# Optimization experiments

Measured on AMD Instinct MI355X. Metric: run time of the kernel, lower is better.

Reference implementation:

```python
import jax, jax.numpy as jnp
import numpy as np

KSIZE = 9
SIGMA = 7.0
ALPHA = 0.05
POOL = 7


def _conv(x, w, pad):
    # x: (N, Cin, H, W), w: (Cout, Cin, kh, kw), zero padding, stride 1
    return jax.lax.conv_general_dilated(
        x, w, window_strides=(1, 1), padding=[(pad, pad), (pad, pad)],
        dimension_numbers=("NCHW", "OIHW", "NCHW"))


def setup_inputs() -> dict:
    key = jax.random.key(0)
    x = jax.random.normal(key, (4, 1, 2048, 2048), dtype=jnp.float32)
    # Sobel filters (ImageGradientsLayer): out ch 0 = Ix, out ch 1 = Iy
    sobel_w = jnp.array(
        [[[[-1., 0., 1.], [-2., 0., 2.], [-1., 0., 1.]]],
         [[[-1., -2., -1.], [0., 0., 0.], [1., 2., 1.]]]], dtype=jnp.float32)
    # Normalized 2D Gaussian kernel, ksize=9, sigma=7
    ax = np.arange(KSIZE) - (KSIZE - 1) / 2.0
    g1 = np.exp(-(ax ** 2) / (2.0 * SIGMA ** 2))
    g2 = np.outer(g1, g1)
    g2 = g2 / g2.sum()
    gauss_w = jnp.asarray(g2, dtype=jnp.float32)[None, None]  # (1,1,9,9)
    return {"x": x, "sobel_w": sobel_w, "gauss_w": gauss_w}


def reference(x, sobel_w, gauss_w):
    # 1) ImageGradientsLayer: Sobel conv -> (N, 2, H, W)
    g = _conv(x, sobel_w, 1)
    Ix, Iy = g[:, 0], g[:, 1]
    # 2) ChannelProductLayer: I_xx, I_yy, I_xy -> (N, 3, H, W)
    prods = jnp.stack([Ix * Ix, Iy * Iy, Ix * Iy], axis=1)
    # 3) SecondMomentMatrixLayer: same 9x9 Gaussian on each channel
    N, C, H, W = prods.shape
    S = _conv(prods.reshape(N * C, 1, H, W), gauss_w, (KSIZE - 1) // 2)
    S = S.reshape(N, C, H, W)
    # 4) CornerResponseLayer: R = det - alpha * trace^2
    det = S[:, 0] * S[:, 1] - S[:, 2] * S[:, 2]
    tr = S[:, 0] + S[:, 1]
    R = (det - ALPHA * tr * tr)[:, None]  # (N, 1, H, W)
    # 5) NMSLayer: global (lower) median threshold, 7x7 maxpool, equality mask
    n = R.size
    med = jnp.sort(R.reshape(-1))[(n - 1) // 2]  # torch.median = lower median
    xt = jnp.where(R > med, R, jnp.zeros_like(R))
    pad = (POOL - 1) // 2
    y = jax.lax.reduce_window(
        xt, -jnp.inf, jax.lax.max, (1, 1, POOL, POOL), (1, 1, 1, 1),
        [(0, 0), (0, 0), (pad, pad), (pad, pad)])
    mask = (xt == y).astype(xt.dtype)
    return mask * xt
```

## Files before the change

### kernel.cpp

```cpp
#include <hip/hip_runtime.h>
#include <cstdint>
#include <math.h>

#define IMH 2048
#define IMW 2048
#define NB 4
#define NPIX (NB*IMH*IMW)
#define MEDRANK ((NPIX-1)/2)
#define ALPHA 0.05f

#define TW 64
#define TH 32

__device__ __forceinline__ uint32_t fkey(float f){
  uint32_t u = __float_as_uint(f);
  return (u & 0x80000000u) ? ~u : (u | 0x80000000u);
}

__device__ __forceinline__ float ldz(const float* __restrict__ p, int r, int c){
  return (r >= 0 && r < IMH && c >= 0 && c < IMW) ? p[(size_t)r*IMW + c] : 0.f;
}

__global__ __launch_bounds__(256) void front_kernel(
    const float* __restrict__ x, const float* __restrict__ sobel_w,
    const float* __restrict__ gauss_w, float* __restrict__ R)
{
  __shared__ float xs[TH+10][TW+16];
  __shared__ float ps[3][TH+8][TW+16];
  __shared__ float hs[TH+8][TW];

  const int tid = threadIdx.x;
  const int C0 = blockIdx.x * TW;
  const int R0 = blockIdx.y * TH;
  const int n  = blockIdx.z;
  const float* xb = x + (size_t)n * (size_t)(IMH*IMW);

  float w0[9], w1[9];
#pragma unroll
  for (int i = 0; i < 9; i++){ w0[i] = sobel_w[i]; w1[i] = sobel_w[9+i]; }
  float ga[9];
  {
    float a4 = sqrtf(gauss_w[4*9+4]);
#pragma unroll
    for (int i = 0; i < 9; i++) ga[i] = gauss_w[4*9+i] / a4;
  }

  for (int u = tid; u < (TH+10)*20; u += 256){
    int r  = u / 20, c4 = u % 20;
    int gr = R0 - 5 + r;
    int gc = C0 - 8 + c4*4;
    float4 v;
    if (gr >= 0 && gr < IMH && gc >= 0 && gc + 3 < IMW){
      v = *reinterpret_cast<const float4*>(&xb[(size_t)gr*IMW + gc]);
    } else {
      v.x = ldz(xb, gr, gc+0);
      v.y = ldz(xb, gr, gc+1);
      v.z = ldz(xb, gr, gc+2);
      v.w = ldz(xb, gr, gc+3);
    }
    *reinterpret_cast<float4*>(&xs[r][c4*4]) = v;
  }
  __syncthreads();

  for (int u = tid; u < (TH+8)*18; u += 256){
    int r  = u / 18;
    int c4 = u % 18 + 1;
    int cb = c4*4;
    int gr = R0 - 4 + r;
    float rw[3][12];
#pragma unroll
    for (int i = 0; i < 3; i++){
      float4 a = *reinterpret_cast<const float4*>(&xs[r+i][cb-4]);
      float4 b = *reinterpret_cast<const float4*>(&xs[r+i][cb]);
      float4 c = *reinterpret_cast<const float4*>(&xs[r+i][cb+4]);
      rw[i][0]=a.x; rw[i][1]=a.y; rw[i][2]=a.z; rw[i][3]=a.w;
      rw[i][4]=b.x; rw[i][5]=b.y; rw[i][6]=b.z; rw[i][7]=b.w;
      rw[i][8]=c.x; rw[i][9]=c.y; rw[i][10]=c.z; rw[i][11]=c.w;
    }
    float o0[4], o1[4], o2[4];
#pragma unroll
    for (int j = 0; j < 4; j++){
      int gc = C0 - 8 + cb + j;
      float ix = 0.f, iy = 0.f;
#pragma unroll
      for (int i = 0; i < 3; i++){
#pragma unroll
        for (int d = 0; d < 3; d++){
          float xv = rw[i][3 + j + d];
          ix = fmaf(w0[i*3+d], xv, ix);
          iy = fmaf(w1[i*3+d], xv, iy);
        }
      }
      bool valid = (gr >= 0 && gr < IMH && gc >= 0 && gc < IMW);
      o0[j] = valid ? ix*ix : 0.f;
      o1[j] = valid ? iy*iy : 0.f;
      o2[j] = valid ? ix*iy : 0.f;
    }
    *reinterpret_cast<float4*>(&ps[0][r][cb]) = make_float4(o0[0],o0[1],o0[2],o0[3]);
    *reinterpret_cast<float4*>(&ps[1][r][cb]) = make_float4(o1[0],o1[1],o1[2],o1[3]);
    *reinterpret_cast<float4*>(&ps[2][r][cb]) = make_float4(o2[0],o2[1],o2[2],o2[3]);
  }
  __syncthreads();

  const int c4o = tid & 15;
  const int r0o = (tid >> 4) * 2;
  float4 sA[3], sB[3];

#pragma unroll
  for (int p = 0; p < 3; p++){
    for (int u = tid; u < (TH+8)*16; u += 256){
      int r  = u / 16, c4 = u % 16;
      float4 t0 = *reinterpret_cast<const float4*>(&ps[p][r][c4*4+4]);
      float4 t1 = *reinterpret_cast<const float4*>(&ps[p][r][c4*4+8]);
      float4 t2 = *reinterpret_cast<const float4*>(&ps[p][r][c4*4+12]);
      float w[12];
      w[0]=t0.x; w[1]=t0.y; w[2]=t0.z; w[3]=t0.w;
      w[4]=t1.x; w[5]=t1.y; w[6]=t1.z; w[7]=t1.w;
      w[8]=t2.x; w[9]=t2.y; w[10]=t2.z; w[11]=t2.w;
      float o[4];
#pragma unroll
      for (int j = 0; j < 4; j++){
        float s = 0.f;
#pragma unroll
        for (int k = 0; k < 9; k++) s = fmaf(ga[k], w[j+k], s);
        o[j] = s;
      }
      *reinterpret_cast<float4*>(&hs[r][c4*4]) = make_float4(o[0],o[1],o[2],o[3]);
    }
    __syncthreads();
    {
      float4 a0 = make_float4(0,0,0,0), a1 = make_float4(0,0,0,0);
#pragma unroll
      for (int k = 0; k < 10; k++){
        float4 hv = *reinterpret_cast<const float4*>(&hs[r0o+k][c4o*4]);
        if (k < 9){
          a0.x = fmaf(ga[k], hv.x, a0.x); a0.y = fmaf(ga[k], hv.y, a0.y);
          a0.z = fmaf(ga[k], hv.z, a0.z); a0.w = fmaf(ga[k], hv.w, a0.w);
        }
        if (k >= 1){
          a1.x = fmaf(ga[k-1], hv.x, a1.x); a1.y = fmaf(ga[k-1], hv.y, a1.y);
          a1.z = fmaf(ga[k-1], hv.z, a1.z); a1.w = fmaf(ga[k-1], hv.w, a1.w);
        }
      }
      sA[p] = a0; sB[p] = a1;
    }
    __syncthreads();
  }

  float* Rb = R + (size_t)n * (size_t)(IMH*IMW);
  {
    float4 o0, o1;
    {
      float s0, s1, s2, det, tr;
      s0=sA[0].x; s1=sA[1].x; s2=sA[2].x; det=s0*s1-s2*s2; tr=s0+s1; o0.x=det-ALPHA*tr*tr;
      s0=sA[0].y; s1=sA[1].y; s2=sA[2].y; det=s0*s1-s2*s2; tr=s0+s1; o0.y=det-ALPHA*tr*tr;
      s0=sA[0].z; s1=sA[1].z; s2=sA[2].z; det=s0*s1-s2*s2; tr=s0+s1; o0.z=det-ALPHA*tr*tr;
      s0=sA[0].w; s1=sA[1].w; s2=sA[2].w; det=s0*s1-s2*s2; tr=s0+s1; o0.w=det-ALPHA*tr*tr;
      s0=sB[0].x; s1=sB[1].x; s2=sB[2].x; det=s0*s1-s2*s2; tr=s0+s1; o1.x=det-ALPHA*tr*tr;
      s0=sB[0].y; s1=sB[1].y; s2=sB[2].y; det=s0*s1-s2*s2; tr=s0+s1; o1.y=det-ALPHA*tr*tr;
      s0=sB[0].z; s1=sB[1].z; s2=sB[2].z; det=s0*s1-s2*s2; tr=s0+s1; o1.z=det-ALPHA*tr*tr;
      s0=sB[0].w; s1=sB[1].w; s2=sB[2].w; det=s0*s1-s2*s2; tr=s0+s1; o1.w=det-ALPHA*tr*tr;
    }
    int orow = R0 + r0o;
    int ocol = C0 + c4o*4;
    *reinterpret_cast<float4*>(&Rb[(size_t)orow*IMW + ocol])     = o0;
    *reinterpret_cast<float4*>(&Rb[(size_t)(orow+1)*IMW + ocol]) = o1;
  }
}

__global__ __launch_bounds__(256) void hist8_kernel(
    const float4* __restrict__ R4, uint32_t* __restrict__ h)
{
  __shared__ uint32_t lh[256];
  lh[threadIdx.x] = 0;
  __syncthreads();
  const int stride = gridDim.x * 256;
  for (int i = blockIdx.x*256 + threadIdx.x; i < NPIX/4; i += stride){
    float4 v = R4[i];
    atomicAdd(&lh[fkey(v.x) >> 24], 1u);
    atomicAdd(&lh[fkey(v.y) >> 24], 1u);
    atomicAdd(&lh[fkey(v.z) >> 24], 1u);
    atomicAdd(&lh[fkey(v.w) >> 24], 1u);
  }
  __syncthreads();
  if (lh[threadIdx.x]) atomicAdd(&h[threadIdx.x], lh[threadIdx.x]);
}

__global__ __launch_bounds__(256) void hist12_kernel(
    const float4* __restrict__ R4, uint32_t* __restrict__ h,
    const uint32_t* __restrict__ state, int phase)
{
  __shared__ uint32_t lh[4096];
  for (int i = threadIdx.x; i < 4096; i += 256) lh[i] = 0;
  __syncthreads();
  const uint32_t target = (phase == 0) ? state[0] : ((state[0] << 12) | state[2]);
  const int shift = (phase == 0) ? 24 : 12;
  const int stride = gridDim.x * 256;
  for (int i = blockIdx.x*256 + threadIdx.x; i < NPIX/4; i += stride){
    float4 v = R4[i];
    uint32_t k;
    k = fkey(v.x); if ((k >> shift) == target) atomicAdd(&lh[(k >> (shift-12)) & 0xfffu], 1u);
    k = fkey(v.y); if ((k >> shift) == target) atomicAdd(&lh[(k >> (shift-12)) & 0xfffu], 1u);
    k = fkey(v.z); if ((k >> shift) == target) atomicAdd(&lh[(k >> (shift-12)) & 0xfffu], 1u);
    k = fkey(v.w); if ((k >> shift) == target) atomicAdd(&lh[(k >> (shift-12)) & 0xfffu], 1u);
  }
  __syncthreads();
  for (int i = threadIdx.x; i < 4096; i += 256)
    if (lh[i]) atomicAdd(&h[i], lh[i]);
}

__global__ __launch_bounds__(256) void select_kernel(
    const uint32_t* __restrict__ h, uint32_t* __restrict__ state,
    int nbins, int phase)
{
  __shared__ uint32_t sc[256];
  const int t = threadIdx.x;
  const int chunk = nbins >> 8;
  uint32_t lsum = 0;
  for (int i = 0; i < chunk; i++) lsum += h[t*chunk + i];
  sc[t] = lsum;
  __syncthreads();
  for (int off = 1; off < 256; off <<= 1){
    uint32_t v = (t >= off) ? sc[t-off] : 0u;
    __syncthreads();
    sc[t] += v;
    __syncthreads();
  }
  const uint32_t excl = sc[t] - lsum;
  const uint32_t rank = (phase == 0) ? (uint32_t)MEDRANK : state[(phase == 1) ? 1 : 3];
  if (rank >= excl && rank < excl + lsum){
    uint32_t cum = excl;
    for (int i = 0; i < chunk; i++){
      uint32_t c = h[t*chunk + i];
      if (rank < cum + c){
        uint32_t bin = (uint32_t)(t*chunk + i);
        if (phase == 0){ state[0] = bin; state[1] = rank - cum; }
        else if (phase == 1){ state[2] = bin; state[3] = rank - cum; }
        else {
          uint32_t key = (state[0] << 24) | (state[2] << 12) | bin;
          uint32_t u = (key & 0x80000000u) ? (key & 0x7fffffffu) : ~key;
          state[4] = u;
        }
        break;
      }
      cum += c;
    }
  }
}

#define PT 64
__global__ __launch_bounds__(256) void nms_kernel(
    const float* __restrict__ R, const uint32_t* __restrict__ state,
    float* __restrict__ out)
{
  __shared__ float xt[PT+6][PT+8];
  __shared__ float hm[PT+6][PT];

  const int tid = threadIdx.x;
  const int C0 = blockIdx.x * PT;
  const int R0 = blockIdx.y * PT;
  const int n  = blockIdx.z;
  const float med = __uint_as_float(state[4]);
  const float* Rb = R + (size_t)n * (size_t)(IMH*IMW);

  for (int u = tid; u < 70*18; u += 256){
    int r  = u / 18, c4 = u % 18;
    int gr = R0 - 3 + r;
    int gc = C0 - 4 + c4*4;
    float4 v;
    if (gr >= 0 && gr < IMH && gc >= 0 && gc + 3 < IMW){
      v = *reinterpret_cast<const float4*>(&Rb[(size_t)gr*IMW + gc]);
      v.x = v.x > med ? v.x : 0.f;
      v.y = v.y > med ? v.y : 0.f;
      v.z = v.z > med ? v.z : 0.f;
      v.w = v.w > med ? v.w : 0.f;
    } else {
      float t0, t1, t2, t3;
      t0 = (gr>=0&&gr<IMH&&gc+0>=0&&gc+0<IMW) ? Rb[(size_t)gr*IMW+gc+0] : -INFINITY;
      t1 = (gr>=0&&gr<IMH&&gc+1>=0&&gc+1<IMW) ? Rb[(size_t)gr*IMW+gc+1] : -INFINITY;
      t2 = (gr>=0&&gr<IMH&&gc+2>=0&&gc+2<IMW) ? Rb[(size_t)gr*IMW+gc+2] : -INFINITY;
      t3 = (gr>=0&&gr<IMH&&gc+3>=0&&gc+3<IMW) ? Rb[(size_t)gr*IMW+gc+3] : -INFINITY;
      v.x = (t0 == -INFINITY) ? t0 : (t0 > med ? t0 : 0.f);
      v.y = (t1 == -INFINITY) ? t1 : (t1 > med ? t1 : 0.f);
      v.z = (t2 == -INFINITY) ? t2 : (t2 > med ? t2 : 0.f);
      v.w = (t3 == -INFINITY) ? t3 : (t3 > med ? t3 : 0.f);
    }
    *reinterpret_cast<float4*>(&xt[r][c4*4]) = v;
  }
  __syncthreads();

  for (int u = tid; u < 70*16; u += 256){
    int r = u / 16, c4 = u % 16;
    float4 t0 = *reinterpret_cast<const float4*>(&xt[r][c4*4]);
    float4 t1 = *reinterpret_cast<const float4*>(&xt[r][c4*4+4]);
    float4 t2 = *reinterpret_cast<const float4*>(&xt[r][c4*4+8]);
    float w[12];
    w[0]=t0.x; w[1]=t0.y; w[2]=t0.z; w[3]=t0.w;
    w[4]=t1.x; w[5]=t1.y; w[6]=t1.z; w[7]=t1.w;
    w[8]=t2.x; w[9]=t2.y; w[10]=t2.z; w[11]=t2.w;
    float o[4];
#pragma unroll
    for (int j = 0; j < 4; j++){
      float m = w[j+1];
#pragma unroll
      for (int k = 2; k <= 7; k++) m = fmaxf(m, w[j+k]);
      o[j] = m;
    }
    *reinterpret_cast<float4*>(&hm[r][c4*4]) = make_float4(o[0],o[1],o[2],o[3]);
  }
  __syncthreads();

  const int c4o = tid & 15;
  const int r0o = (tid >> 4) * 4;
  float4 hv[10];
#pragma unroll
  for (int k = 0; k < 10; k++)
    hv[k] = *reinterpret_cast<const float4*>(&hm[r0o+k][c4o*4]);

  float* ob = out + (size_t)n * (size_t)(IMH*IMW);
#pragma unroll
  for (int i = 0; i < 4; i++){
    float4 y = hv[i];
#pragma unroll
    for (int k = 1; k < 7; k++){
      float4 t = hv[i+k];
      y.x = fmaxf(y.x, t.x); y.y = fmaxf(y.y, t.y);
      y.z = fmaxf(y.z, t.z); y.w = fmaxf(y.w, t.w);
    }
    float4 c = *reinterpret_cast<const float4*>(&xt[r0o+i+3][c4o*4+4]);
    float4 o;
    o.x = (c.x == y.x) ? c.x : 0.f;
    o.y = (c.y == y.y) ? c.y : 0.f;
    o.z = (c.z == y.z) ? c.z : 0.f;
    o.w = (c.w == y.w) ? c.w : 0.f;
    *reinterpret_cast<float4*>(&ob[(size_t)(R0+r0o+i)*IMW + C0 + c4o*4]) = o;
  }
}

extern "C" void kernel_launch(void* const* d_in, const int* in_sizes, int n_in,
                              void* d_out, int out_size, void* d_ws, size_t ws_size,
                              hipStream_t stream)
{
  (void)in_sizes; (void)n_in; (void)out_size; (void)ws_size;
  const float* x  = (const float*)d_in[0];
  const float* sw = (const float*)d_in[1];
  const float* gw = (const float*)d_in[2];
  float* out = (float*)d_out;

  float* R = (float*)d_ws;
  uint32_t* hist = (uint32_t*)((char*)d_ws + (size_t)NPIX * sizeof(float));
  uint32_t* h8    = hist;
  uint32_t* h12a  = hist + 256;
  uint32_t* h12b  = hist + 256 + 4096;
  uint32_t* state = hist + 256 + 4096 + 4096;

  hipMemsetAsync(hist, 0, (256 + 4096 + 4096) * sizeof(uint32_t), stream);

  front_kernel<<<dim3(IMW/TW, IMH/TH, NB), 256, 0, stream>>>(x, sw, gw, R);

  hist8_kernel <<<1024, 256, 0, stream>>>((const float4*)R, h8);
  select_kernel<<<1,    256, 0, stream>>>(h8, state, 256, 0);
  hist12_kernel<<<1024, 256, 0, stream>>>((const float4*)R, h12a, state, 0);
  select_kernel<<<1,    256, 0, stream>>>(h12a, state, 4096, 1);
  hist12_kernel<<<1024, 256, 0, stream>>>((const float4*)R, h12b, state, 1);
  select_kernel<<<1,    256, 0, stream>>>(h12b, state, 4096, 2);

  nms_kernel<<<dim3(IMW/PT, IMH/PT, NB), 256, 0, stream>>>(R, state, out);
}
```

Before: 363.1 us.

## Fuse Sobel and horizontal Gaussian pass, replicate histogram bins, pad LDS rows

```diff
diff --git a/kernel.cpp b/kernel.cpp
--- a/kernel.cpp
+++ b/kernel.cpp
@@ -25,9 +25,8 @@
     const float* __restrict__ x, const float* __restrict__ sobel_w,
     const float* __restrict__ gauss_w, float* __restrict__ R)
 {
-  __shared__ float xs[TH+10][TW+16];
-  __shared__ float ps[3][TH+8][TW+16];
-  __shared__ float hs[TH+8][TW];
+  __shared__ float xs[TH+10][84];
+  __shared__ float hs[3][TH+8][68];
 
   const int tid = threadIdx.x;
   const int C0 = blockIdx.x * TW;
@@ -62,105 +61,91 @@
   }
   __syncthreads();
 
-  for (int u = tid; u < (TH+8)*18; u += 256){
-    int r  = u / 18;
-    int c4 = u % 18 + 1;
-    int cb = c4*4;
-    int gr = R0 - 4 + r;
-    float rw[3][12];
+  for (int u = tid; u < (TH+8)*16; u += 256){
+    int hr = u >> 4;
+    int oc = (u & 15) * 4;
+    int gr = R0 - 4 + hr;
+    bool rowv = ((unsigned)gr < (unsigned)IMH);
+
+    float ix[12], iy[12];
+#pragma unroll
+    for (int j = 0; j < 12; j++){ ix[j] = 0.f; iy[j] = 0.f; }
 #pragma unroll
     for (int i = 0; i < 3; i++){
-      float4 a = *reinterpret_cast<const float4*>(&xs[r+i][cb-4]);
-      float4 b = *reinterpret_cast<const float4*>(&xs[r+i][cb]);
-      float4 c = *reinterpret_cast<const float4*>(&xs[r+i][cb+4]);
-      rw[i][0]=a.x; rw[i][1]=a.y; rw[i][2]=a.z; rw[i][3]=a.w;
-      rw[i][4]=b.x; rw[i][5]=b.y; rw[i][6]=b.z; rw[i][7]=b.w;
-      rw[i][8]=c.x; rw[i][9]=c.y; rw[i][10]=c.z; rw[i][11]=c.w;
-    }
-    float o0[4], o1[4], o2[4];
-#pragma unroll
-    for (int j = 0; j < 4; j++){
-      int gc = C0 - 8 + cb + j;
-      float ix = 0.f, iy = 0.f;
-#pragma unroll
-      for (int i = 0; i < 3; i++){
+      float xr[20];
+#pragma unroll
+      for (int m = 0; m < 5; m++){
+        float4 t = *reinterpret_cast<const float4*>(&xs[hr+i][oc + m*4]);
+        xr[m*4+0]=t.x; xr[m*4+1]=t.y; xr[m*4+2]=t.z; xr[m*4+3]=t.w;
+      }
+#pragma unroll
+      for (int j = 0; j < 12; j++){
 #pragma unroll
         for (int d = 0; d < 3; d++){
-          float xv = rw[i][3 + j + d];
-          ix = fmaf(w0[i*3+d], xv, ix);
-          iy = fmaf(w1[i*3+d], xv, iy);
+          float xv = xr[3 + j + d];
+          ix[j] = fmaf(w0[i*3+d], xv, ix[j]);
+          iy[j] = fmaf(w1[i*3+d], xv, iy[j]);
         }
       }
-      bool valid = (gr >= 0 && gr < IMH && gc >= 0 && gc < IMW);
-      o0[j] = valid ? ix*ix : 0.f;
-      o1[j] = valid ? iy*iy : 0.f;
-      o2[j] = valid ? ix*iy : 0.f;
-    }
-    *reinterpret_cast<float4*>(&ps[0][r][cb]) = make_float4(o0[0],o0[1],o0[2],o0[3]);
-    *reinterpret_cast<float4*>(&ps[1][r][cb]) = make_float4(o1[0],o1[1],o1[2],o1[3]);
-    *reinterpret_cast<float4*>(&ps[2][r][cb]) = make_float4(o2[0],o2[1],o2[2],o2[3]);
+    }
+    float pr[3][12];
+#pragma unroll
+    for (int j = 0; j < 12; j++){
+      int gc = C0 + oc - 4 + j;
+      bool v = rowv && ((unsigned)gc < (unsigned)IMW);
+      float a = v ? ix[j] : 0.f;
+      float b = v ? iy[j] : 0.f;
+      pr[0][j] = a*a; pr[1][j] = b*b; pr[2][j] = a*b;
+    }
+#pragma unroll
+    for (int p = 0; p < 3; p++){
+      float o[4];
+#pragma unroll
+      for (int jj = 0; jj < 4; jj++){
+        float s = 0.f;
+#pragma unroll
+        for (int k = 0; k < 9; k++) s = fmaf(ga[k], pr[p][jj+k], s);
+        o[jj] = s;
+      }
+      *reinterpret_cast<float4*>(&hs[p][hr][oc]) = make_float4(o[0],o[1],o[2],o[3]);
+    }
   }
   __syncthreads();
 
   const int c4o = tid & 15;
   const int r0o = (tid >> 4) * 2;
   float4 sA[3], sB[3];
-
 #pragma unroll
   for (int p = 0; p < 3; p++){
-    for (int u = tid; u < (TH+8)*16; u += 256){
-      int r  = u / 16, c4 = u % 16;
-      float4 t0 = *reinterpret_cast<const float4*>(&ps[p][r][c4*4+4]);
-      float4 t1 = *reinterpret_cast<const float4*>(&ps[p][r][c4*4+8]);
-      float4 t2 = *reinterpret_cast<const float4*>(&ps[p][r][c4*4+12]);
-      float w[12];
-      w[0]=t0.x; w[1]=t0.y; w[2]=t0.z; w[3]=t0.w;
-      w[4]=t1.x; w[5]=t1.y; w[6]=t1.z; w[7]=t1.w;
-      w[8]=t2.x; w[9]=t2.y; w[10]=t2.z; w[11]=t2.w;
-      float o[4];
-#pragma unroll
-      for (int j = 0; j < 4; j++){
-        float s = 0.f;
-#pragma unroll
-        for (int k = 0; k < 9; k++) s = fmaf(ga[k], w[j+k], s);
-        o[j] = s;
-      }
-      *reinterpret_cast<float4*>(&hs[r][c4*4]) = make_float4(o[0],o[1],o[2],o[3]);
-    }
-    __syncthreads();
-    {
-      float4 a0 = make_float4(0,0,0,0), a1 = make_float4(0,0,0,0);
-#pragma unroll
-      for (int k = 0; k < 10; k++){
-        float4 hv = *reinterpret_cast<const float4*>(&hs[r0o+k][c4o*4]);
-        if (k < 9){
-          a0.x = fmaf(ga[k], hv.x, a0.x); a0.y = fmaf(ga[k], hv.y, a0.y);
-          a0.z = fmaf(ga[k], hv.z, a0.z); a0.w = fmaf(ga[k], hv.w, a0.w);
-        }
-        if (k >= 1){
-          a1.x = fmaf(ga[k-1], hv.x, a1.x); a1.y = fmaf(ga[k-1], hv.y, a1.y);
-          a1.z = fmaf(ga[k-1], hv.z, a1.z); a1.w = fmaf(ga[k-1], hv.w, a1.w);
-        }
-      }
-      sA[p] = a0; sB[p] = a1;
-    }
-    __syncthreads();
+    float4 a0 = make_float4(0,0,0,0), a1 = make_float4(0,0,0,0);
+#pragma unroll
+    for (int k = 0; k < 10; k++){
+      float4 hv = *reinterpret_cast<const float4*>(&hs[p][r0o+k][c4o*4]);
+      if (k < 9){
+        a0.x = fmaf(ga[k], hv.x, a0.x); a0.y = fmaf(ga[k], hv.y, a0.y);
+        a0.z = fmaf(ga[k], hv.z, a0.z); a0.w = fmaf(ga[k], hv.w, a0.w);
+      }
+      if (k >= 1){
+        a1.x = fmaf(ga[k-1], hv.x, a1.x); a1.y = fmaf(ga[k-1], hv.y, a1.y);
+        a1.z = fmaf(ga[k-1], hv.z, a1.z); a1.w = fmaf(ga[k-1], hv.w, a1.w);
+      }
+    }
+    sA[p] = a0; sB[p] = a1;
   }
 
   float* Rb = R + (size_t)n * (size_t)(IMH*IMW);
   {
     float4 o0, o1;
-    {
-      float s0, s1, s2, det, tr;
-      s0=sA[0].x; s1=sA[1].x; s2=sA[2].x; det=s0*s1-s2*s2; tr=s0+s1; o0.x=det-ALPHA*tr*tr;
-      s0=sA[0].y; s1=sA[1].y; s2=sA[2].y; det=s0*s1-s2*s2; tr=s0+s1; o0.y=det-ALPHA*tr*tr;
-      s0=sA[0].z; s1=sA[1].z; s2=sA[2].z; det=s0*s1-s2*s2; tr=s0+s1; o0.z=det-ALPHA*tr*tr;
-      s0=sA[0].w; s1=sA[1].w; s2=sA[2].w; det=s0*s1-s2*s2; tr=s0+s1; o0.w=det-ALPHA*tr*tr;
-      s0=sB[0].x; s1=sB[1].x; s2=sB[2].x; det=s0*s1-s2*s2; tr=s0+s1; o1.x=det-ALPHA*tr*tr;
-      s0=sB[0].y; s1=sB[1].y; s2=sB[2].y; det=s0*s1-s2*s2; tr=s0+s1; o1.y=det-ALPHA*tr*tr;
-      s0=sB[0].z; s1=sB[1].z; s2=sB[2].z; det=s0*s1-s2*s2; tr=s0+s1; o1.z=det-ALPHA*tr*tr;
-      s0=sB[0].w; s1=sB[1].w; s2=sB[2].w; det=s0*s1-s2*s2; tr=s0+s1; o1.w=det-ALPHA*tr*tr;
-    }
+    float s0, s1, s2, det, tr;
+    s0=sA[0].x; s1=sA[1].x; s2=sA[2].x; det=s0*s1-s2*s2; tr=s0+s1; o0.x=det-ALPHA*tr*tr;
+    s0=sA[0].y; s1=sA[1].y; s2=sA[2].y; det=s0*s1-s2*s2; tr=s0+s1; o0.y=det-ALPHA*tr*tr;
+    s0=sA[0].z; s1=sA[1].z; s2=sA[2].z; det=s0*s1-s2*s2; tr=s0+s1; o0.z=det-ALPHA*tr*tr;
+    s0=sA[0].w; s1=sA[1].w; s2=sA[2].w; det=s0*s1-s2*s2; tr=s0+s1; o0.w=det-ALPHA*tr*tr;
+    s0=sB[0].x; s1=sB[1].x; s2=sB[2].x; det=s0*s1-s2*s2; tr=s0+s1; o1.x=det-ALPHA*tr*tr;
+    s0=sB[0].y; s1=sB[1].y; s2=sB[2].y; det=s0*s1-s2*s2; tr=s0+s1; o1.y=det-ALPHA*tr*tr;
+    s0=sB[0].z; s1=sB[1].z; s2=sB[2].z; det=s0*s1-s2*s2; tr=s0+s1; o1.z=det-ALPHA*tr*tr;
+    s0=sB[0].w; s1=sB[1].w; s2=sB[2].w; det=s0*s1-s2*s2; tr=s0+s1; o1.w=det-ALPHA*tr*tr;
+
     int orow = R0 + r0o;
     int ocol = C0 + c4o*4;
     *reinterpret_cast<float4*>(&Rb[(size_t)orow*IMW + ocol])     = o0;
@@ -171,19 +156,26 @@
 __global__ __launch_bounds__(256) void hist8_kernel(
     const float4* __restrict__ R4, uint32_t* __restrict__ h)
 {
-  __shared__ uint32_t lh[256];
-  lh[threadIdx.x] = 0;
-  __syncthreads();
+  __shared__ uint32_t lh[256*32];
+  for (int i = threadIdx.x; i < 256*32; i += 256) lh[i] = 0;
+  __syncthreads();
+  const int copy = threadIdx.x & 31;
   const int stride = gridDim.x * 256;
   for (int i = blockIdx.x*256 + threadIdx.x; i < NPIX/4; i += stride){
     float4 v = R4[i];
-    atomicAdd(&lh[fkey(v.x) >> 24], 1u);
-    atomicAdd(&lh[fkey(v.y) >> 24], 1u);
-    atomicAdd(&lh[fkey(v.z) >> 24], 1u);
-    atomicAdd(&lh[fkey(v.w) >> 24], 1u);
-  }
-  __syncthreads();
-  if (lh[threadIdx.x]) atomicAdd(&h[threadIdx.x], lh[threadIdx.x]);
+    atomicAdd(&lh[(fkey(v.x) >> 24)*32 + copy], 1u);
+    atomicAdd(&lh[(fkey(v.y) >> 24)*32 + copy], 1u);
+    atomicAdd(&lh[(fkey(v.z) >> 24)*32 + copy], 1u);
+    atomicAdd(&lh[(fkey(v.w) >> 24)*32 + copy], 1u);
+  }
+  __syncthreads();
+  {
+    const int t = threadIdx.x;
+    uint32_t s = 0;
+#pragma unroll
+    for (int i = 0; i < 32; i++) s += lh[t*32 + ((t + i) & 31)];
+    if (s) atomicAdd(&h[t], s);
+  }
 }
 
 __global__ __launch_bounds__(256) void hist12_kernel(
@@ -253,8 +245,8 @@
     const float* __restrict__ R, const uint32_t* __restrict__ state,
     float* __restrict__ out)
 {
-  __shared__ float xt[PT+6][PT+8];
-  __shared__ float hm[PT+6][PT];
+  __shared__ float xt[PT+6][76];
+  __shared__ float hm[PT+6][68];
 
   const int tid = threadIdx.x;
   const int C0 = blockIdx.x * PT;
```

Result: faster. 303.6 us (-16.4%).
